# Performance work log

Hardware: AMD Instinct MI355X
Metric: run time of the kernel (lower is better)

## Reference

```python
import jax, jax.numpy as jnp
import numpy as np

N_DIMS = 8
N_REGIMES = 8
CAPACITY = 16
KERNEL = 2
DILATIONS = (1, 2, 4, 8)
BOTTLE = (32, 32, 32, 32)
B = 128
T_LEN = 512
N_STEPS = T_LEN - CAPACITY


def setup_inputs() -> dict:
    key = jax.random.key(0)
    ks = jax.random.split(key, 8)
    x = jax.random.normal(ks[0], (B, N_DIMS, T_LEN), jnp.float32)
    temp = jnp.ones((), jnp.float32)
    u = jax.random.uniform(ks[1], (N_STEPS, B, 1, N_REGIMES), jnp.float32)

    def mkw(k, o, i):
        return jax.random.normal(k, (o, i, KERNEL), jnp.float32) / np.float32(np.sqrt(i * KERNEL))

    c_in = N_DIMS + N_REGIMES
    w0 = mkw(ks[2], BOTTLE[0], c_in)
    b0 = jnp.zeros((BOTTLE[0],), jnp.float32)
    w1 = mkw(ks[3], BOTTLE[1], BOTTLE[0])
    b1 = jnp.zeros((BOTTLE[1],), jnp.float32)
    w2 = mkw(ks[4], BOTTLE[2], BOTTLE[1])
    b2 = jnp.zeros((BOTTLE[2],), jnp.float32)
    w3 = mkw(ks[5], N_REGIMES, BOTTLE[3])
    b3 = jnp.zeros((N_REGIMES,), jnp.float32)
    return {"x": x, "temp": temp, "u": u, "w0": w0, "b0": b0, "w1": w1,
            "b1": b1, "w2": w2, "b2": b2, "w3": w3, "b3": b3, "T": T_LEN}


def _conv(h, w, b, d):
    # causal dilated conv1d, VALID padding (windowing handles causality)
    out = jax.lax.conv_general_dilated(h, w, (1,), 'VALID', rhs_dilation=(d,),
                                       dimension_numbers=('NCH', 'OIH', 'NCH'))
    return out + b[None, :, None]


def _forward(x, temp, u, params, T):
    cap = CAPACITY
    pad = sum(DILATIONS)  # F.pad(x, (sum(dilations), 0)) -> left-pad time axis
    xpad = jnp.pad(x, ((0, 0), (0, 0), (pad, 0)))
    n_steps = T - cap
    # windows x_pad[:, :, t-cap:t] for t in [cap, T) -> (n_steps, B, D, cap)
    idx = jnp.arange(n_steps)[:, None] + jnp.arange(cap)[None, :]
    xw = jnp.transpose(xpad[:, :, idx], (2, 0, 1, 3))
    g = -jnp.log(-jnp.log(u + 1e-10) + 1e-10)  # Gumbel(0,1) noise
    Bn = x.shape[0]
    K = u.shape[-1]
    z0 = jnp.zeros((Bn, K, cap), x.dtype)  # capacity initial zero regimes
    layers = tuple(zip(params[0::2], params[1::2], DILATIONS))

    def step(zbuf, inp):
        xw_t, g_t = inp  # (B, D, cap), (B, 1, K)
        h = jnp.concatenate([xw_t, zbuf], axis=1)  # (B, D+K, cap)
        for (w, b, d) in layers:
            h = jax.nn.elu(_conv(h, w, b, d))
        logq = jax.nn.log_softmax(h[:, :, -1], axis=1)  # (B, K)
        y = jax.nn.softmax((logq + g_t[:, 0, :]) / temp, axis=-1)  # gumbel-softmax sample
        zbuf = jnp.concatenate([zbuf[:, :, 1:], y[:, :, None]], axis=2)
        return zbuf, (y, logq)

    _, (zs, logqs) = jax.lax.scan(step, z0, (xw, g))
    z_all = jnp.concatenate([z0, jnp.transpose(zs, (1, 2, 0))], axis=2)  # (B, K, T)
    logq_out = jnp.transpose(logqs, (1, 2, 0))[..., None]  # (B, K, n_steps, 1) = torch.stack(dim=2)
    return z_all, logq_out


def reference(x, temp, u, w0, b0, w1, b1, w2, b2, w3, b3, T):
    return _forward(x, temp, u, (w0, b0, w1, b1, w2, b2, w3, b3), T)
```

## Files before the change

### kernel.cpp

```cpp
#include <hip/hip_runtime.h>

#define NB      128
#define ND      8
#define NK      8
#define TLEN    512
#define NSTEPS  496

#define INVLN2f 1.44269504088896340736f

__device__ __forceinline__ float fexp(float x) { return __expf(x); }
__device__ __forceinline__ float flog(float x) { return __logf(x); }
__device__ __forceinline__ float frcp(float x) { return __builtin_amdgcn_rcpf(x); }
__device__ __forceinline__ float elur(float x) { return x > 0.f ? x : fexp(x) - 1.f; }

#if defined(__has_builtin)
#if __has_builtin(__builtin_amdgcn_exp2f)
#define fexp2(x) __builtin_amdgcn_exp2f(x)
#endif
#endif
#ifndef fexp2
#define fexp2(x) exp2f(x)
#endif

#define DPP_ROR4(v) __int_as_float(__builtin_amdgcn_mov_dpp(__float_as_int(v), 0x124, 0xF, 0xF, false))
#define DPP_X1(v)   __int_as_float(__builtin_amdgcn_mov_dpp(__float_as_int(v), 0xB1, 0xF, 0xF, false))
#define DPP_X2(v)   __int_as_float(__builtin_amdgcn_mov_dpp(__float_as_int(v), 0x4E, 0xF, 0xF, false))
#define DPP_RORN(v, ctrl) __int_as_float(__builtin_amdgcn_mov_dpp(__float_as_int(v), (ctrl), 0xF, 0xF, false))

#define RED8_MAX(m) { m = fmaxf(m, DPP_X1(m)); m = fmaxf(m, DPP_X2(m)); m = fmaxf(m, DPP_ROR4(m)); }
#define RED8_SUM(s) { s = s + DPP_X1(s); s = s + DPP_X2(s); s = s + DPP_ROR4(s); }

typedef unsigned int uint2v __attribute__((ext_vector_type(2)));
typedef float floatx2 __attribute__((ext_vector_type(2)));

__device__ __forceinline__ floatx2 f2(float t) { floatx2 r; r.x = t; r.y = t; return r; }

#if defined(__has_builtin)
#if __has_builtin(__builtin_amdgcn_permlane32_swap)
#define HAVE_PLSWAP 1
#endif
#if __has_builtin(__builtin_amdgcn_permlane16_swap)
#define HAVE_PL16SWAP 1
#endif
#endif

#ifdef HAVE_PLSWAP
__device__ __forceinline__ float xhalfsum(float v) {
    unsigned int u = __float_as_uint(v);
    uint2v r = __builtin_amdgcn_permlane32_swap(u, u, false, false);
    return __uint_as_float(r[0]) + __uint_as_float(r[1]);
}
#else
__device__ __forceinline__ float xhalfsum(float v) { return v + __shfl_xor(v, 32); }
#endif

#ifdef HAVE_PL16SWAP
#define TOB(v) ({                                                                  \
    float _v = (v);                                                                \
    unsigned _u = __float_as_uint(_v);                                             \
    uint2v _r = __builtin_amdgcn_permlane16_swap(_u, _u, false, false);            \
    float _o = __uint_as_float(selr0 ? _r[0] : _r[1]);                             \
    (lane < 32) ? _v : _o; })
#else
#define TOB(v) ({                                                                  \
    float _v = (v);                                                                \
    float _o = __uint_as_float((unsigned)__builtin_amdgcn_ds_swizzle(              \
                   (int)__float_as_uint(_v), 0x401F));                             \
    (lane < 32) ? _v : _o; })
#endif

__device__ __forceinline__ floatx2 rotdot16x2p(float vB, const floatx2* __restrict__ wp) {
    float t1 = DPP_RORN(vB, 0x121), t2 = DPP_RORN(vB, 0x122), t3 = DPP_RORN(vB, 0x123);
    float t4 = DPP_RORN(vB, 0x124), t5 = DPP_RORN(vB, 0x125), t6 = DPP_RORN(vB, 0x126);
    float t7 = DPP_RORN(vB, 0x127), t8 = DPP_RORN(vB, 0x128), t9 = DPP_RORN(vB, 0x129);
    float tA = DPP_RORN(vB, 0x12A), tB = DPP_RORN(vB, 0x12B), tC = DPP_RORN(vB, 0x12C);
    float tD = DPP_RORN(vB, 0x12D), tE = DPP_RORN(vB, 0x12E), tF = DPP_RORN(vB, 0x12F);
    floatx2 a0 = wp[0] * f2(vB);
    floatx2 a1 = wp[1] * f2(t1);
    floatx2 a2 = wp[2] * f2(t2);
    floatx2 a3 = wp[3] * f2(t3);
    a0 = __builtin_elementwise_fma(wp[4],  f2(t4), a0);
    a1 = __builtin_elementwise_fma(wp[5],  f2(t5), a1);
    a2 = __builtin_elementwise_fma(wp[6],  f2(t6), a2);
    a3 = __builtin_elementwise_fma(wp[7],  f2(t7), a3);
    a0 = __builtin_elementwise_fma(wp[8],  f2(t8), a0);
    a1 = __builtin_elementwise_fma(wp[9],  f2(t9), a1);
    a2 = __builtin_elementwise_fma(wp[10], f2(tA), a2);
    a3 = __builtin_elementwise_fma(wp[11], f2(tB), a3);
    a0 = __builtin_elementwise_fma(wp[12], f2(tC), a0);
    a1 = __builtin_elementwise_fma(wp[13], f2(tD), a1);
    a2 = __builtin_elementwise_fma(wp[14], f2(tE), a2);
    a3 = __builtin_elementwise_fma(wp[15], f2(tF), a3);
    return (a0 + a1) + (a2 + a3);
}

#define STEP(qv, S1, S2, S3, DO_OUT)                                              \
  {                                                                               \
    const int q_ = (qv);                                                          \
    float g2_own = 0.f;                                                           \
    if (DO_OUT) g2_own = gls[(q_ - 15) * NK + o3];                                \
    const float4* _xq = (const float4*)&xcol[q_ + tap][0];                        \
    float4 _xa = _xq[0], _xb = _xq[1];                                            \
                               \
    float o0v = elur(XZ);                                                         \
                                                                     \
    float v0B = TOB(o0v);                                                         \
    floatx2 d1 = rotdot16x2p(v0B, w1p);                                           \
    float o1v = elur(xhalfsum(d1.x + P1[S1]));                                    \
    P1[S1] = b1h + d1.y;                                                          \
                                                                     \
    float v1B = TOB(o1v);                                                         \
    floatx2 d2 = rotdot16x2p(v1B, w2p);                                           \
    float o2v = elur(xhalfsum(d2.x + P2[S2]));                                    \
    P2[S2] = b2h + d2.y;                                                          \
                                                                     \
    float v2B = TOB(o2v);                                                         \
    floatx2 d3 = rotdot16x2p(v2B, w3p);                                           \
    float a3m = elur(xhalfsum(d3.x + P3[S3]));                                    \
    P3[S3] = b3h + d3.y;                                                          \
    if (DO_OUT) {                                                                 \
                            \
      float F = fexp2(fmaf(a3m, klog, g2_own));                                   \
      float S = F; RED8_SUM(S);                                                   \
      float r2 = frcp(S);                                                         \
            \
      float rt1 = DPP_RORN(F, 0x121), rt2 = DPP_RORN(F, 0x122);                   \
      float rt3 = DPP_RORN(F, 0x123), rt4 = DPP_RORN(F, 0x124);                   \
      float rt5 = DPP_RORN(F, 0x125), rt6 = DPP_RORN(F, 0x126);                   \
      float rt7 = DPP_RORN(F, 0x127);                                             \
      float na = wznrot[0] * F,   nb = wznrot[1] * rt1;                           \
      float nc = wznrot[2] * rt2, nd = wznrot[3] * rt3;                           \
      na = fmaf(wznrot[4], rt4, na); nb = fmaf(wznrot[5], rt5, nb);               \
      nc = fmaf(wznrot[6], rt6, nc); nd = fmaf(wznrot[7], rt7, nd);               \
      float oa = wzorot[0] * F,   ob = wzorot[1] * rt1;                           \
      float oc = wzorot[2] * rt2, od = wzorot[3] * rt3;                           \
      oa = fmaf(wzorot[4], rt4, oa); ob = fmaf(wzorot[5], rt5, ob);               \
      oc = fmaf(wzorot[6], rt6, oc); od = fmaf(wzorot[7], rt7, od);               \
      ZN   = ((na + nb) + (nc + nd)) * r2;             \
      ZQ2n = ((oa + ob) + (oc + od)) * r2;             \
                                                \
      float mx = a3m; RED8_MAX(mx);                                               \
      float e = fexp(a3m - mx);                                                   \
      float se = e; RED8_SUM(se);                                                 \
      float lse = mx + flog(se);                                                  \
      if (lane < 8) {                                                             \
        outg[zoff + lane * TLEN + q_ + 1]       = F * r2;                         \
        outg[qoff + lane * NSTEPS + (q_ - 15)]  = a3m - lse;                      \
      }                                                                           \
    }                                                                             \
             \
    {                                                                             \
      float s0 = fmaf(wxr[0], _xa.x, fmaf(wxr[1], _xa.y, 0.f));                   \
      float s1 = fmaf(wxr[2], _xa.z, fmaf(wxr[3], _xa.w, 0.f));                   \
      float s2 = fmaf(wxr[4], _xb.x, fmaf(wxr[5], _xb.y, 0.f));                   \
      float s3 = fmaf(wxr[6], _xb.z, fmaf(wxr[7], _xb.w, 0.f));                   \
      float xp = (s0 + s1) + (s2 + s3);                                           \
      XZ = (xhalfsum(xp) + b0r + ZQ2) + ZN;                                       \
      ZQ2 = ZQ2n;                                                                 \
    }                                                                             \
  }

__global__ __launch_bounds__(64, 1)
void regime_scan_kernel(const float* __restrict__ xg,
                        const float* __restrict__ tempg,
                        const float* __restrict__ ug,
                        const float* __restrict__ w0g,
                        const float* __restrict__ b0g,
                        const float* __restrict__ w1g,
                        const float* __restrict__ b1g,
                        const float* __restrict__ w2g,
                        const float* __restrict__ b2g,
                        const float* __restrict__ w3g,
                        const float* __restrict__ b3g,
                        float* __restrict__ outg)
{
    __shared__ __align__(16) float xcol[527][8];
    __shared__ __align__(16) float gls[NSTEPS * NK];

    const int lane = threadIdx.x;
    const int b    = blockIdx.x;
    const int c    = lane & 31;
    const int o3   = lane & 7;
    const int tap  = (lane < 32) ? 1 : 0;
    const int s    = lane & 15;
    const int rowq = lane >> 4;
    const int jbase = ((rowq ^ (rowq >> 1)) & 1) << 4;

    int dir;
    {
        int l15 = lane & 15;
        int rr1 = __builtin_amdgcn_mov_dpp(l15, 0x121, 0xF, 0xF, false);
        dir = (rr1 == ((l15 + 1) & 15)) ? 1 : -1;
    }
    int selr0 = 0;
#ifdef HAVE_PL16SWAP
    {
        unsigned li = (unsigned)lane;
        uint2v pr = __builtin_amdgcn_permlane16_swap(li, li, false, false);
        selr0 = (pr[0] == (li ^ 16u)) ? 1 : 0;
    }
#endif

    float wznrot[8], wzorot[8];
    #pragma unroll
    for (int r = 0; r < 8; ++r) {
        int ch = (o3 + dir * r) & 7;
        wznrot[r] = w0g[c * 32 + (8 + ch) * 2 + 1];
        wzorot[r] = w0g[c * 32 + (8 + ch) * 2 + 0];
    }
    float wxr[8];
    #pragma unroll
    for (int d = 0; d < 8; ++d) wxr[d] = w0g[c * 32 + d * 2 + tap];
    floatx2 w1p[16], w2p[16], w3p[16];
    #pragma unroll
    for (int r = 0; r < 16; ++r) {
        int jj = jbase + ((s + dir * r) & 15);
        w1p[r].x = w1g[c  * 64 + jj * 2 + 1];
        w1p[r].y = w1g[c  * 64 + jj * 2 + 0];
        w2p[r].x = w2g[c  * 64 + jj * 2 + 1];
        w2p[r].y = w2g[c  * 64 + jj * 2 + 0];
        w3p[r].x = w3g[o3 * 64 + jj * 2 + 1];
        w3p[r].y = w3g[o3 * 64 + jj * 2 + 0];
    }
    const float b0r  = b0g[c];
    const float b1h  = 0.5f * b1g[c];
    const float b2h  = 0.5f * b2g[c];
    const float b3h  = 0.5f * b3g[o3];
    const float tinv = frcp(tempg[0]);
    const float klog = tinv * INVLN2f;

    if (lane < 15) {
        #pragma unroll
        for (int d = 0; d < ND; ++d) xcol[lane][d] = 0.f;
    }
    const float* xb = xg + b * (ND * TLEN);
    for (int t = lane; t < TLEN; t += 64) {
        #pragma unroll
        for (int d = 0; d < ND; ++d) xcol[15 + t][d] = xb[d * TLEN + t];
    }
    for (int idx = lane; idx < NSTEPS * NK; idx += 64) {
        int st = idx >> 3, k = idx & 7;
        float uu = ug[st * (NB * NK) + b * NK + k];
        float g  = -flog(-flog(uu + 1e-10f) + 1e-10f);
        gls[idx] = g * klog;
    }
    const int zoff = b * (NK * TLEN);
    const int qoff = NB * NK * TLEN + b * (NK * NSTEPS);
    for (int idx = lane; idx < NK * 16; idx += 64) {
        outg[zoff + (idx >> 4) * TLEN + (idx & 15)] = 0.f;
    }

    float P1[2] = { b1h, b1h };
    float P2[4] = { b2h, b2h, b2h, b2h };
    float P3[8];
    #pragma unroll
    for (int k = 0; k < 8; ++k) P3[k] = b3h;
    float ZQ2 = 0.f, ZQ2n = 0.f, ZN = 0.f;
    float XZ;
    {
        const float4* xq = (const float4*)&xcol[tap][0];
        float4 xa = xq[0], xbv = xq[1];
        float s0 = fmaf(wxr[0], xa.x, fmaf(wxr[1], xa.y, 0.f));
        float s1 = fmaf(wxr[2], xa.z, fmaf(wxr[3], xa.w, 0.f));
        float s2 = fmaf(wxr[4], xbv.x, fmaf(wxr[5], xbv.y, 0.f));
        float s3 = fmaf(wxr[6], xbv.z, fmaf(wxr[7], xbv.w, 0.f));
        XZ = xhalfsum((s0 + s1) + (s2 + s3)) + b0r;
    }

    #pragma unroll
    for (int q = 1; q <= 14; ++q) STEP(q, q & 1, q & 3, q & 7, 0);

    for (int qb = 15; qb <= 503; qb += 8) {
        #pragma unroll
        for (int u = 0; u < 8; ++u) {
            STEP(qb + u, (15 + u) & 1, (15 + u) & 3, (15 + u) & 7, 1);
        }
    }
}

extern "C" void kernel_launch(void* const* d_in, const int* in_sizes, int n_in,
                              void* d_out, int out_size, void* d_ws, size_t ws_size,
                              hipStream_t stream) {
    (void)in_sizes; (void)n_in; (void)out_size; (void)d_ws; (void)ws_size;
    regime_scan_kernel<<<dim3(NB), dim3(64), 0, stream>>>(
        (const float*)d_in[0],
        (const float*)d_in[1],
        (const float*)d_in[2],
        (const float*)d_in[3],
        (const float*)d_in[4],
        (const float*)d_in[5],
        (const float*)d_in[6],
        (const float*)d_in[7],
        (const float*)d_in[8],
        (const float*)d_in[9],
        (const float*)d_in[10],
        (float*)d_out);
}
```

Before: 360.7 us.

## Pack eight batch wavefronts per block and stream inputs through per-wave LDS rings

Each block now hosts eight independent wavefronts, one per batch element, and launches 16 blocks instead of 128 single-wave blocks. The full x column and Gumbel table per batch no longer sit in LDS. Each wave keeps an 80-row x ring and a 64-step noise window, refilled every 64 steps inside the sequential scan. This shrinks LDS per wave so several waves can share a CU, but it leaves only 16 CUs busy and adds global loads and log work in the middle of the serial chain.

```diff
diff --git a/kernel.cpp b/kernel.cpp
--- a/kernel.cpp
+++ b/kernel.cpp
@@ -5,6 +5,8 @@
 #define NK      8
 #define TLEN    512
 #define NSTEPS  496
+#define WPB     8
+#define XRING   80
 
 #define INVLN2f 1.44269504088896340736f
 
@@ -94,12 +96,12 @@
     return (a0 + a1) + (a2 + a3);
 }
 
-#define STEP(qv, S1, S2, S3, DO_OUT)                                              \
+#define STEP(qv, LOFFv, S1, S2, S3, DO_OUT)                                       \
   {                                                                               \
     const int q_ = (qv);                                                          \
     float g2_own = 0.f;                                                           \
-    if (DO_OUT) g2_own = gls[(q_ - 15) * NK + o3];                                \
-    const float4* _xq = (const float4*)&xcol[q_ + tap][0];                        \
+    if (DO_OUT) g2_own = gw[(((q_) - 15) & 63) * NK + o3];                        \
+    const float4* _xq = (const float4*)&xw[((LOFFv) + tap) * 8];                  \
     float4 _xa = _xq[0], _xb = _xq[1];                                            \
                                \
     float o0v = elur(XZ);                                                         \
@@ -160,7 +162,7 @@
     }                                                                             \
   }
 
-__global__ __launch_bounds__(64, 1)
+__global__ __launch_bounds__(512, 2)
 void regime_scan_kernel(const float* __restrict__ xg,
                         const float* __restrict__ tempg,
                         const float* __restrict__ ug,
@@ -174,17 +176,21 @@
                         const float* __restrict__ b3g,
                         float* __restrict__ outg)
 {
-    __shared__ __align__(16) float xcol[527][8];
-    __shared__ __align__(16) float gls[NSTEPS * NK];
-
-    const int lane = threadIdx.x;
-    const int b    = blockIdx.x;
+    __shared__ __align__(16) float xbuf[WPB][XRING][8];
+    __shared__ __align__(16) float glsw[WPB][64 * NK];
+
+    const int lane = threadIdx.x & 63;
+    const int wid  = threadIdx.x >> 6;
+    const int b    = blockIdx.x * WPB + wid;
     const int c    = lane & 31;
     const int o3   = lane & 7;
     const int tap  = (lane < 32) ? 1 : 0;
     const int s    = lane & 15;
     const int rowq = lane >> 4;
     const int jbase = ((rowq ^ (rowq >> 1)) & 1) << 4;
+
+    float* xw = &xbuf[wid][0][0];
+    float* gw = &glsw[wid][0];
 
     int dir;
     {
@@ -229,20 +235,16 @@
     const float tinv = frcp(tempg[0]);
     const float klog = tinv * INVLN2f;
 
-    if (lane < 15) {
-        #pragma unroll
-        for (int d = 0; d < ND; ++d) xcol[lane][d] = 0.f;
-    }
     const float* xb = xg + b * (ND * TLEN);
-    for (int t = lane; t < TLEN; t += 64) {
-        #pragma unroll
-        for (int d = 0; d < ND; ++d) xcol[15 + t][d] = xb[d * TLEN + t];
-    }
-    for (int idx = lane; idx < NSTEPS * NK; idx += 64) {
+    for (int idx = lane; idx < XRING * ND; idx += 64) {
+        int lc = idx >> 3, d = idx & 7;
+        int t = lc - 15;
+        xw[idx] = (t >= 0) ? xb[d * TLEN + t] : 0.f;
+    }
+    for (int idx = lane; idx < 64 * NK; idx += 64) {
         int st = idx >> 3, k = idx & 7;
         float uu = ug[st * (NB * NK) + b * NK + k];
-        float g  = -flog(-flog(uu + 1e-10f) + 1e-10f);
-        gls[idx] = g * klog;
+        gw[idx] = -flog(-flog(uu + 1e-10f) + 1e-10f) * klog;
     }
     const int zoff = b * (NK * TLEN);
     const int qoff = NB * NK * TLEN + b * (NK * NSTEPS);
@@ -258,7 +260,7 @@
     float ZQ2 = 0.f, ZQ2n = 0.f, ZN = 0.f;
     float XZ;
     {
-        const float4* xq = (const float4*)&xcol[tap][0];
+        const float4* xq = (const float4*)&xw[tap * 8];
         float4 xa = xq[0], xbv = xq[1];
         float s0 = fmaf(wxr[0], xa.x, fmaf(wxr[1], xa.y, 0.f));
         float s1 = fmaf(wxr[2], xa.z, fmaf(wxr[3], xa.w, 0.f));
@@ -268,12 +270,36 @@
     }
 
     #pragma unroll
-    for (int q = 1; q <= 14; ++q) STEP(q, q & 1, q & 3, q & 7, 0);
-
-    for (int qb = 15; qb <= 503; qb += 8) {
-        #pragma unroll
-        for (int u = 0; u < 8; ++u) {
-            STEP(qb + u, (15 + u) & 1, (15 + u) & 3, (15 + u) & 7, 1);
+    for (int q = 1; q <= 14; ++q) STEP(q, q, q & 1, q & 3, q & 7, 0);
+
+    for (int chk = 0; chk < 8; ++chk) {
+        const int B0 = 15 + chk * 64;
+        if (chk > 0) {
+            for (int idx = lane; idx < 65 * ND; idx += 64) {
+                int lc = idx >> 3, d = idx & 7;
+                int t = B0 + lc - 15;
+                xw[idx] = (t < TLEN) ? xb[d * TLEN + t] : 0.f;
+            }
+            const int c0 = chk * 64;
+            for (int idx = lane; idx < 64 * NK; idx += 64) {
+                int st = c0 + (idx >> 3), k = idx & 7;
+                float g2v = 0.f;
+                if (st < NSTEPS) {
+                    float uu = ug[st * (NB * NK) + b * NK + k];
+                    g2v = -flog(-flog(uu + 1e-10f) + 1e-10f) * klog;
+                }
+                gw[idx] = g2v;
+            }
+        }
+        const int jmax = (chk == 7) ? 6 : 8;
+        const int lb   = (chk == 0) ? 15 : 0;
+        for (int j = 0; j < jmax; ++j) {
+            const int q0 = B0 + j * 8;
+            const int l0 = lb + j * 8;
+            #pragma unroll
+            for (int u = 0; u < 8; ++u) {
+                STEP(q0 + u, l0 + u, (15 + u) & 1, (15 + u) & 3, (15 + u) & 7, 1);
+            }
         }
     }
 }
@@ -282,7 +308,7 @@
                               void* d_out, int out_size, void* d_ws, size_t ws_size,
                               hipStream_t stream) {
     (void)in_sizes; (void)n_in; (void)out_size; (void)d_ws; (void)ws_size;
-    regime_scan_kernel<<<dim3(NB), dim3(64), 0, stream>>>(
+    regime_scan_kernel<<<dim3(NB / WPB), dim3(WPB * 64), 0, stream>>>(
         (const float*)d_in[0],
         (const float*)d_in[1],
         (const float*)d_in[2],
```

Measured after the change: 589.3 us. +63.4%, slower.

## Split scan into critical-path wave and helper wave for outputs and prefetch

Applied to the files above, without the earlier changes.

Launches two waves per batch item. Wave 0 runs only the serial recurrence and writes each step's pre-softmax activation to a shared ring. Wave 1 precomputes the layer-0 x-projection and Gumbel noise in double-buffered 64-step chunks, then computes log-softmax and writes the z and logq outputs one block of 8 steps behind. This takes the log-softmax and global stores off the recurrence's critical path. In exchange it adds a block barrier every 8 steps and duplicates the softmax exp/reduction in the helper wave.

```diff
diff --git a/kernel.cpp b/kernel.cpp
--- a/kernel.cpp
+++ b/kernel.cpp
@@ -94,36 +94,28 @@
     return (a0 + a1) + (a2 + a3);
 }
 
-#define STEP(qv, S1, S2, S3, DO_OUT)                                              \
+#define STEP0(qv, S1, S2, S3, DO_OUT, XPEXPR)                                     \
   {                                                                               \
     const int q_ = (qv);                                                          \
-    float g2_own = 0.f;                                                           \
-    if (DO_OUT) g2_own = gls[(q_ - 15) * NK + o3];                                \
-    const float4* _xq = (const float4*)&xcol[q_ + tap][0];                        \
-    float4 _xa = _xq[0], _xb = _xq[1];                                            \
-                               \
     float o0v = elur(XZ);                                                         \
-                                                                     \
     float v0B = TOB(o0v);                                                         \
     floatx2 d1 = rotdot16x2p(v0B, w1p);                                           \
     float o1v = elur(xhalfsum(d1.x + P1[S1]));                                    \
     P1[S1] = b1h + d1.y;                                                          \
-                                                                     \
     float v1B = TOB(o1v);                                                         \
     floatx2 d2 = rotdot16x2p(v1B, w2p);                                           \
     float o2v = elur(xhalfsum(d2.x + P2[S2]));                                    \
     P2[S2] = b2h + d2.y;                                                          \
-                                                                     \
     float v2B = TOB(o2v);                                                         \
     floatx2 d3 = rotdot16x2p(v2B, w3p);                                           \
     float a3m = elur(xhalfsum(d3.x + P3[S3]));                                    \
     P3[S3] = b3h + d3.y;                                                          \
     if (DO_OUT) {                                                                 \
-                            \
+      amring[(q_) & 15][lane] = a3m;                                              \
+      float g2_own = XGg[((q_ - 15) >> 6) & 1][(q_ - 15) & 63][o3];               \
       float F = fexp2(fmaf(a3m, klog, g2_own));                                   \
       float S = F; RED8_SUM(S);                                                   \
       float r2 = frcp(S);                                                         \
-            \
       float rt1 = DPP_RORN(F, 0x121), rt2 = DPP_RORN(F, 0x122);                   \
       float rt3 = DPP_RORN(F, 0x123), rt4 = DPP_RORN(F, 0x124);                   \
       float rt5 = DPP_RORN(F, 0x125), rt6 = DPP_RORN(F, 0x126);                   \
@@ -136,31 +128,32 @@
       float oc = wzorot[2] * rt2, od = wzorot[3] * rt3;                           \
       oa = fmaf(wzorot[4], rt4, oa); ob = fmaf(wzorot[5], rt5, ob);               \
       oc = fmaf(wzorot[6], rt6, oc); od = fmaf(wzorot[7], rt7, od);               \
-      ZN   = ((na + nb) + (nc + nd)) * r2;             \
-      ZQ2n = ((oa + ob) + (oc + od)) * r2;             \
-                                                \
-      float mx = a3m; RED8_MAX(mx);                                               \
-      float e = fexp(a3m - mx);                                                   \
-      float se = e; RED8_SUM(se);                                                 \
-      float lse = mx + flog(se);                                                  \
-      if (lane < 8) {                                                             \
-        outg[zoff + lane * TLEN + q_ + 1]       = F * r2;                         \
-        outg[qoff + lane * NSTEPS + (q_ - 15)]  = a3m - lse;                      \
-      }                                                                           \
+      ZN   = ((na + nb) + (nc + nd)) * r2;                                        \
+      ZQ2n = ((oa + ob) + (oc + od)) * r2;                                        \
     }                                                                             \
-             \
-    {                                                                             \
-      float s0 = fmaf(wxr[0], _xa.x, fmaf(wxr[1], _xa.y, 0.f));                   \
-      float s1 = fmaf(wxr[2], _xa.z, fmaf(wxr[3], _xa.w, 0.f));                   \
-      float s2 = fmaf(wxr[4], _xb.x, fmaf(wxr[5], _xb.y, 0.f));                   \
-      float s3 = fmaf(wxr[6], _xb.z, fmaf(wxr[7], _xb.w, 0.f));                   \
-      float xp = (s0 + s1) + (s2 + s3);                                           \
-      XZ = (xhalfsum(xp) + b0r + ZQ2) + ZN;                                       \
-      ZQ2 = ZQ2n;                                                                 \
+    XZ = ((XPEXPR) + ZQ2) + ZN;                                                   \
+    ZQ2 = ZQ2n;                                                                   \
+  }
+
+#define ROLEA(pv)                                                                 \
+  {                                                                               \
+    const int p_ = (pv);                                                          \
+    float a3 = amring[(p_) & 15][lane];                                           \
+    float g2 = XGg[((p_ - 15) >> 6) & 1][(p_ - 15) & 63][o3];                     \
+    float F = fexp2(fmaf(a3, klog, g2));                                          \
+    float S = F; RED8_SUM(S);                                                     \
+    float r2 = frcp(S);                                                           \
+    float mx = a3; RED8_MAX(mx);                                                  \
+    float e = fexp(a3 - mx);                                                      \
+    float se = e; RED8_SUM(se);                                                   \
+    float lse = mx + flog(se);                                                    \
+    if (lane < 8) {                                                               \
+      outg[zoff + lane * TLEN + p_ + 1]       = F * r2;                           \
+      outg[qoff + lane * NSTEPS + (p_ - 15)]  = a3 - lse;                         \
     }                                                                             \
   }
 
-__global__ __launch_bounds__(64, 1)
+__global__ __launch_bounds__(128, 1)
 void regime_scan_kernel(const float* __restrict__ xg,
                         const float* __restrict__ tempg,
                         const float* __restrict__ ug,
@@ -174,10 +167,14 @@
                         const float* __restrict__ b3g,
                         float* __restrict__ outg)
 {
-    __shared__ __align__(16) float xcol[527][8];
-    __shared__ __align__(16) float gls[NSTEPS * NK];
-
-    const int lane = threadIdx.x;
+    __shared__ __align__(16) float xring[80 * 8];
+    __shared__ __align__(16) float XGx[2][64][32];
+    __shared__ __align__(16) float XGg[2][64][8];
+    __shared__ __align__(16) float XPwarm[15][32];
+    __shared__ __align__(16) float amring[16][64];
+
+    const int lane = threadIdx.x & 63;
+    const int wid  = threadIdx.x >> 6;
     const int b    = blockIdx.x;
     const int c    = lane & 31;
     const int o3   = lane & 7;
@@ -201,79 +198,140 @@
     }
 #endif
 
-    float wznrot[8], wzorot[8];
-    #pragma unroll
-    for (int r = 0; r < 8; ++r) {
-        int ch = (o3 + dir * r) & 7;
-        wznrot[r] = w0g[c * 32 + (8 + ch) * 2 + 1];
-        wzorot[r] = w0g[c * 32 + (8 + ch) * 2 + 0];
-    }
-    float wxr[8];
-    #pragma unroll
-    for (int d = 0; d < 8; ++d) wxr[d] = w0g[c * 32 + d * 2 + tap];
-    floatx2 w1p[16], w2p[16], w3p[16];
-    #pragma unroll
-    for (int r = 0; r < 16; ++r) {
-        int jj = jbase + ((s + dir * r) & 15);
-        w1p[r].x = w1g[c  * 64 + jj * 2 + 1];
-        w1p[r].y = w1g[c  * 64 + jj * 2 + 0];
-        w2p[r].x = w2g[c  * 64 + jj * 2 + 1];
-        w2p[r].y = w2g[c  * 64 + jj * 2 + 0];
-        w3p[r].x = w3g[o3 * 64 + jj * 2 + 1];
-        w3p[r].y = w3g[o3 * 64 + jj * 2 + 0];
-    }
-    const float b0r  = b0g[c];
-    const float b1h  = 0.5f * b1g[c];
-    const float b2h  = 0.5f * b2g[c];
-    const float b3h  = 0.5f * b3g[o3];
     const float tinv = frcp(tempg[0]);
     const float klog = tinv * INVLN2f;
-
-    if (lane < 15) {
-        #pragma unroll
-        for (int d = 0; d < ND; ++d) xcol[lane][d] = 0.f;
-    }
-    const float* xb = xg + b * (ND * TLEN);
-    for (int t = lane; t < TLEN; t += 64) {
-        #pragma unroll
-        for (int d = 0; d < ND; ++d) xcol[15 + t][d] = xb[d * TLEN + t];
-    }
-    for (int idx = lane; idx < NSTEPS * NK; idx += 64) {
-        int st = idx >> 3, k = idx & 7;
-        float uu = ug[st * (NB * NK) + b * NK + k];
-        float g  = -flog(-flog(uu + 1e-10f) + 1e-10f);
-        gls[idx] = g * klog;
-    }
     const int zoff = b * (NK * TLEN);
     const int qoff = NB * NK * TLEN + b * (NK * NSTEPS);
-    for (int idx = lane; idx < NK * 16; idx += 64) {
-        outg[zoff + (idx >> 4) * TLEN + (idx & 15)] = 0.f;
-    }
-
-    float P1[2] = { b1h, b1h };
-    float P2[4] = { b2h, b2h, b2h, b2h };
-    float P3[8];
-    #pragma unroll
-    for (int k = 0; k < 8; ++k) P3[k] = b3h;
-    float ZQ2 = 0.f, ZQ2n = 0.f, ZN = 0.f;
-    float XZ;
-    {
-        const float4* xq = (const float4*)&xcol[tap][0];
-        float4 xa = xq[0], xbv = xq[1];
-        float s0 = fmaf(wxr[0], xa.x, fmaf(wxr[1], xa.y, 0.f));
-        float s1 = fmaf(wxr[2], xa.z, fmaf(wxr[3], xa.w, 0.f));
-        float s2 = fmaf(wxr[4], xbv.x, fmaf(wxr[5], xbv.y, 0.f));
-        float s3 = fmaf(wxr[6], xbv.z, fmaf(wxr[7], xbv.w, 0.f));
-        XZ = xhalfsum((s0 + s1) + (s2 + s3)) + b0r;
-    }
-
-    #pragma unroll
-    for (int q = 1; q <= 14; ++q) STEP(q, q & 1, q & 3, q & 7, 0);
-
-    for (int qb = 15; qb <= 503; qb += 8) {
-        #pragma unroll
-        for (int u = 0; u < 8; ++u) {
-            STEP(qb + u, (15 + u) & 1, (15 + u) & 3, (15 + u) & 7, 1);
+
+    if (wid == 0) {
+        float wznrot[8], wzorot[8];
+        #pragma unroll
+        for (int r = 0; r < 8; ++r) {
+            int ch = (o3 + dir * r) & 7;
+            wznrot[r] = w0g[c * 32 + (8 + ch) * 2 + 1];
+            wzorot[r] = w0g[c * 32 + (8 + ch) * 2 + 0];
+        }
+        floatx2 w1p[16], w2p[16], w3p[16];
+        #pragma unroll
+        for (int r = 0; r < 16; ++r) {
+            int jj = jbase + ((s + dir * r) & 15);
+            w1p[r].x = w1g[c  * 64 + jj * 2 + 1];
+            w1p[r].y = w1g[c  * 64 + jj * 2 + 0];
+            w2p[r].x = w2g[c  * 64 + jj * 2 + 1];
+            w2p[r].y = w2g[c  * 64 + jj * 2 + 0];
+            w3p[r].x = w3g[o3 * 64 + jj * 2 + 1];
+            w3p[r].y = w3g[o3 * 64 + jj * 2 + 0];
+        }
+        const float b1h = 0.5f * b1g[c];
+        const float b2h = 0.5f * b2g[c];
+        const float b3h = 0.5f * b3g[o3];
+
+        __syncthreads();
+
+        float P1[2] = { b1h, b1h };
+        float P2[4] = { b2h, b2h, b2h, b2h };
+        float P3[8];
+        #pragma unroll
+        for (int k = 0; k < 8; ++k) P3[k] = b3h;
+        float ZQ2 = 0.f, ZQ2n = 0.f, ZN = 0.f;
+        float XZ = XPwarm[1][c];
+
+        #pragma unroll
+        for (int q = 1; q <= 14; ++q) {
+            STEP0(q, q & 1, q & 3, q & 7, 0,
+                  (q < 14 ? XPwarm[q + 1][c] : XGx[0][0][c]));
+        }
+        __syncthreads();
+
+        for (int j = 0; j < 62; ++j) {
+            const int qb = 15 + 8 * j;
+            #pragma unroll
+            for (int u = 0; u < 8; ++u) {
+                STEP0(qb + u, (15 + u) & 1, (15 + u) & 3, (15 + u) & 7, 1,
+                      XGx[((qb + u - 14) >> 6) & 1][(qb + u - 14) & 63][c]);
+            }
+            __syncthreads();
+        }
+    } else {
+        float wxr[8];
+        #pragma unroll
+        for (int d = 0; d < 8; ++d) wxr[d] = w0g[c * 32 + d * 2 + tap];
+        const float b0r = b0g[c];
+        const float* xb = xg + b * (ND * TLEN);
+
+        for (int idx = lane; idx < 80 * ND; idx += 64) {
+            int l = idx >> 3, d = idx & 7;
+            int t = l - 15;
+            xring[idx] = (t >= 0) ? xb[d * TLEN + t] : 0.f;
+        }
+        for (int it = 0; it <= 77; ++it) {
+            const float4* xq = (const float4*)&xring[(it + tap) * 8];
+            float4 xa = xq[0], xbv = xq[1];
+            float s0 = fmaf(wxr[0], xa.x, fmaf(wxr[1], xa.y, 0.f));
+            float s1 = fmaf(wxr[2], xa.z, fmaf(wxr[3], xa.w, 0.f));
+            float s2 = fmaf(wxr[4], xbv.x, fmaf(wxr[5], xbv.y, 0.f));
+            float s3 = fmaf(wxr[6], xbv.z, fmaf(wxr[7], xbv.w, 0.f));
+            float h = xhalfsum((s0 + s1) + (s2 + s3)) + b0r;
+            if (lane < 32) {
+                if (it < 14) XPwarm[it + 1][c] = h;
+                else         XGx[0][it - 14][c] = h;
+            }
+        }
+        for (int idx = lane; idx < 64 * NK; idx += 64) {
+            int st = idx >> 3, kk = idx & 7;
+            float uu = ug[st * (NB * NK) + b * NK + kk];
+            XGg[0][idx >> 3][kk] = -flog(-flog(uu + 1e-10f) + 1e-10f) * klog;
+        }
+        for (int idx = lane; idx < NK * 16; idx += 64) {
+            outg[zoff + (idx >> 4) * TLEN + (idx & 15)] = 0.f;
+        }
+
+        __syncthreads();
+        __syncthreads();
+
+        for (int j = 0; j < 62; ++j) {
+            if (j >= 1) {
+                const int p0 = 7 + 8 * j;
+                #pragma unroll
+                for (int u = 0; u < 8; ++u) ROLEA(p0 + u);
+            }
+            if ((j & 7) == 0 && j <= 48) {
+                const int cn = (j >> 3) + 1;
+                const int base = 14 + 64 * cn;
+                for (int idx = lane; idx < 66 * ND; idx += 64) {
+                    int l = idx >> 3, d = idx & 7;
+                    int t = base + l - 15;
+                    xring[idx] = (t < TLEN) ? xb[d * TLEN + t] : 0.f;
+                }
+            }
+            if ((j & 7) == 1 && j <= 49) {
+                const int cn = (j >> 3) + 1;
+                const int kb = cn & 1;
+                for (int i = 0; i < 64; ++i) {
+                    const float4* xq = (const float4*)&xring[(i + tap) * 8];
+                    float4 xa = xq[0], xbv = xq[1];
+                    float s0 = fmaf(wxr[0], xa.x, fmaf(wxr[1], xa.y, 0.f));
+                    float s1 = fmaf(wxr[2], xa.z, fmaf(wxr[3], xa.w, 0.f));
+                    float s2 = fmaf(wxr[4], xbv.x, fmaf(wxr[5], xbv.y, 0.f));
+                    float s3 = fmaf(wxr[6], xbv.z, fmaf(wxr[7], xbv.w, 0.f));
+                    float h = xhalfsum((s0 + s1) + (s2 + s3)) + b0r;
+                    if (lane < 32) XGx[kb][i][c] = h;
+                }
+                for (int idx = lane; idx < 64 * NK; idx += 64) {
+                    int st = 64 * cn + (idx >> 3), kk = idx & 7;
+                    float v = 0.f;
+                    if (st < NSTEPS) {
+                        float uu = ug[st * (NB * NK) + b * NK + kk];
+                        v = -flog(-flog(uu + 1e-10f) + 1e-10f) * klog;
+                    }
+                    XGg[kb][idx >> 3][kk] = v;
+                }
+            }
+            __syncthreads();
+        }
+        {
+            #pragma unroll
+            for (int u = 0; u < 8; ++u) ROLEA(503 + u);
         }
     }
 }
@@ -282,7 +340,7 @@
                               void* d_out, int out_size, void* d_ws, size_t ws_size,
                               hipStream_t stream) {
     (void)in_sizes; (void)n_in; (void)out_size; (void)d_ws; (void)ws_size;
-    regime_scan_kernel<<<dim3(NB), dim3(64), 0, stream>>>(
+    regime_scan_kernel<<<dim3(NB), dim3(128), 0, stream>>>(
         (const float*)d_in[0],
         (const float*)d_in[1],
         (const float*)d_in[2],
```

Measured after the change: 360.4 us. No clear change (-0.1%).
